# Kernel tuning notes

Hardware: AMD Instinct MI355X
Metric: run time of the kernel (lower is better)

The kernel has to match this reference:

```python
import jax, jax.numpy as jnp
import numpy as np

B, L, N_EMBD = 4, 2048, 768
N_HIDDEN, N_BINS, V, VOCAB = 32, 8, 64, 1270
TIME_BINS = np.array([0.0, 0.25, 0.5, 1.0, 2.0, 5.0, 10.0, 20.0, 40.0], dtype=np.float32)
TASK_TOKENS = np.arange(5, 5 + 19 * V, 19, dtype=np.int32)  # sorted, all > 0, < VOCAB


def setup_inputs() -> dict:
    key = jax.random.key(0)
    k0, k1, k2, k3, k4, k5 = jax.random.split(key, 6)
    # ages in years, sorted along trajectory; next-event age is slightly later
    age = jnp.sort(jax.random.uniform(k0, (B, L), dtype=jnp.float32) * 80.0, axis=-1)
    targets_age = age + jax.random.uniform(k1, (B, L), dtype=jnp.float32) * 5.0
    targets = jax.random.randint(k2, (B, L), 0, VOCAB, dtype=jnp.int32)
    h = jax.random.normal(k3, (B, L, N_EMBD), dtype=jnp.float32)
    # nn.Linear weights (stored transposed so forward is x @ W)
    W1 = jax.random.normal(k4, (N_EMBD, N_BINS * N_HIDDEN), dtype=jnp.float32) * 0.02
    W2 = jax.random.normal(k5, (N_HIDDEN, V), dtype=jnp.float32) * 0.02
    task_tokens = jnp.asarray(TASK_TOKENS)
    time_bins = jnp.asarray(TIME_BINS)
    return {"h": h, "age": age, "targets_age": targets_age, "targets": targets,
            "W1": W1, "W2": W2, "task_tokens": task_tokens, "time_bins": time_bins}


def reference(h, age, targets_age, targets, W1, W2, task_tokens, time_bins):
    # ---- time_to_event ----
    # delta_t[b, j, k] = targets_age[b, k] - age[b, j]
    delta_t = targets_age[:, None, :] - age[:, :, None]  # (B, L, L)
    # triu token map: keep target token at column k if k >= j, else 0
    jj = jnp.arange(L, dtype=jnp.int32)
    triu_mask = jj[None, :] >= jj[:, None]  # (L, L)
    targets_exp = jnp.where(triu_mask[None], targets[:, None, :], 0)  # (B, L, L)
    # token_map: task token t -> rank+1 in sorted task tokens; others -> 0
    tmap = jnp.zeros((VOCAB,), dtype=jnp.int32).at[task_tokens].set(
        jnp.arange(1, V + 1, dtype=jnp.int32))
    mapped = tmap[targets_exp]  # (B, L, L) values in [0, V]
    # scatter_reduce(amin): for each (b, j, v) find min column k with mapped == v
    seg_base = (jnp.arange(B * L, dtype=jnp.int32) * (V + 1)).reshape(B, L, 1)
    seg_ids = (seg_base + mapped).reshape(-1)
    k_idx = jnp.broadcast_to(jj[None, None, :], (B, L, L)).reshape(-1)
    tok = jax.ops.segment_min(k_idx, seg_ids, num_segments=B * L * (V + 1))
    tok = tok.reshape(B, L, V + 1)[:, :, 1:]  # drop bucket 0 -> (B, L, V)
    no_event = tok >= L  # empty segments fill with int max
    tok = jnp.minimum(tok, L - 1)
    tte = jnp.take_along_axis(delta_t, tok, axis=-1)  # (B, L, V)
    # ---- piecewise_time ----
    last_censor = targets_age[:, -1:] - age  # (B, L)
    starts, ends = time_bins[:-1], time_bins[1:]  # (N_BINS,)
    tte_e = tte[:, :, None, :]  # (B, L, 1, V)
    occur = (tte_e > starts[:, None]) & (tte_e <= ends[:, None]) & (~no_event[:, :, None, :])
    cens = jnp.clip(last_censor[:, :, None, None], 0.0, (ends - starts)[:, None])
    surv_or_event_time = jnp.where(occur, tte_e, cens)  # (B, L, N_BINS, V)
    # ---- head ----
    hh = (h @ W1).reshape(B, L, N_BINS, N_HIDDEN)
    log_lambda = jnp.einsum('blnh,hv->blnv', hh, W2)  # (B, L, N_BINS, V)
    # ---- loss ----
    ll_survival = jnp.mean(-jnp.exp(log_lambda) * surv_or_event_time)
    ll_to_event = jnp.mean(log_lambda * occur.astype(log_lambda.dtype))
    return -(ll_survival + ll_to_event)
```

## Files before the change

### kernel.cpp

```cpp
#include <hip/hip_runtime.h>
#include <hip/hip_bf16.h>

#define B_      4
#define L_      2048
#define NE_     768
#define NOUT_   256
#define NH_     32
#define NB_     8
#define V_      64
#define VOCAB_  1270
#define NC_     32
#define CS_     64
#define BM_     32
#define BK_     32
#define NT_     24
#define DEPTH_  4
#define NROWS_  8192
#define GRID_MAIN_ 256
#define INV_M_  (1.0f / 4194304.0f)
#define INF_    0x7FFFFFFF

typedef float f32x4 __attribute__((ext_vector_type(4)));
typedef short s16x8 __attribute__((ext_vector_type(8)));

__device__ __forceinline__ unsigned short f2bf(float x) {
    union { float f; unsigned u; } c; c.f = x;
    unsigned u = c.u;
    return (unsigned short)((u + 0x7fffu + ((u >> 16) & 1u)) >> 16);
}


__global__ void __launch_bounds__(256)
k_prep(const int* __restrict__ task_tokens, const float* __restrict__ W1,
       const float* __restrict__ W2, const int* __restrict__ targets,
       short* __restrict__ W1t, short* __restrict__ W2t,
       int* __restrict__ mt, int* __restrict__ firstocc, unsigned* __restrict__ cnt) {
    __shared__ float tl[64][67];
    __shared__ int   stask[V_];
    __shared__ int   smt[4][CS_];
    const int tid = threadIdx.x;

    if (blockIdx.x < 48) {
        const int tIdx = blockIdx.x;
        const int kt = (tIdx % 12) * 64;
        const int ct = (tIdx / 12) * 64;
        #pragma unroll
        for (int p = 0; p < 4; ++p) {
            int kk = (tid >> 4) + p * 16;
            int cc = (tid & 15) * 4;
            float4 v = *reinterpret_cast<const float4*>(&W1[(kt + kk) * NOUT_ + ct + cc]);
            tl[kk][cc] = v.x; tl[kk][cc + 1] = v.y; tl[kk][cc + 2] = v.z; tl[kk][cc + 3] = v.w;
        }
        __syncthreads();
        #pragma unroll
        for (int p = 0; p < 8; ++p) {
            int oc  = (tid >> 5) + p * 8;
            int ok2 = (tid & 31) * 2;
            unsigned pk = ((unsigned)f2bf(tl[ok2 + 1][oc]) << 16) | f2bf(tl[ok2][oc]);
            *reinterpret_cast<unsigned*>(&W1t[(ct + oc) * NE_ + kt + ok2]) = pk;
        }
        return;
    }
    if (blockIdx.x == 48) {
        if (tid == 0) cnt[0] = 0u;
        #pragma unroll
        for (int q = 0; q < 8; ++q) {
            int i = tid + q * 256;
            int col = i >> 5, j = i & 31;
            W2t[col * NH_ + j] = (short)f2bf(W2[j * V_ + col]);
        }
        return;
    }
    if (tid < V_) stask[tid] = task_tokens[tid];
    __syncthreads();
    const int gi = tid >> 6;
    const int v  = tid & 63;
    const int g  = (blockIdx.x - 49) * 4 + gi;
    const int b  = g >> 5, c = g & 31;
    int t = targets[b * L_ + c * CS_ + v];
    int mval = -1;
    #pragma unroll
    for (int j = 0; j < V_; ++j)
        mval = (stask[j] == t) ? j : mval;
    mt[b * L_ + c * CS_ + v] = mval;
    smt[gi][v] = mval;
    int first = INF_;
    for (int j = CS_ - 1; j >= 0; --j)
        if (smt[gi][j] == v) first = c * CS_ + j;
    firstocc[(b * NC_ + c) * V_ + v] = first;
}

__global__ void __launch_bounds__(512, 2)
k_main(const float* __restrict__ h, const float* __restrict__ age,
       const float* __restrict__ targets_age,
       const int* __restrict__ mt, const int* __restrict__ firstocc,
       const short* __restrict__ W1t, const short* __restrict__ W2t,
       const float* __restrict__ time_bins, float* __restrict__ partials,
       unsigned* __restrict__ cnt, float* __restrict__ out) {
    __shared__ __align__(16) short sA[2][BM_][40];
    __shared__ __align__(16) short sB[2][256][40];
    __shared__ __align__(16) short sW2[V_][40];
    __shared__ float stte[BM_][66];
    __shared__ int   sminI[8][V_];
    __shared__ int   smt[CS_];
    __shared__ float sage[BM_];
    __shared__ float sred[8];
    __shared__ float s2[4];
    __shared__ int   sLast;

    const int tid = threadIdx.x;
    const int w   = tid >> 6;
    const int l   = tid & 63;
    const int l15 = l & 15;
    const int l4  = l >> 4;
    const int r0  = blockIdx.x * BM_;
    const int b   = r0 >> 11;
    const int pos0 = r0 & (L_ - 1);
    const int c    = pos0 >> 6;
    const int off  = pos0 & 63;

    const int arow = tid >> 4;
    const int akc  = tid & 15;
    const int brow = tid >> 2;
    const int bch  = tid & 3;
    const float* hA  = &h[(r0 + arow) * NE_ + akc * 2];
    const short* bS0 = &W1t[brow * NE_ + bch * 8];
    const short* bS1 = &W1t[(brow + 128) * NE_ + bch * 8];

    float2 aR[DEPTH_];
    s16x8  bR0[DEPTH_], bR1[DEPTH_];
    #pragma unroll
    for (int p = 0; p < DEPTH_; ++p) {
        aR[p]  = *(const float2*)(hA + p * BK_);
        bR0[p] = *(const s16x8*)(bS0 + p * BK_);
        bR1[p] = *(const s16x8*)(bS1 + p * BK_);
    }

    if (tid < CS_)  smt[tid]  = mt[b * L_ + c * CS_ + tid];
    if (tid < BM_)  sage[tid] = age[r0 + tid];
    if (tid < 256) {
        int col = tid >> 2, ch = tid & 3;
        *(s16x8*)&sW2[col][ch * 8] = *(const s16x8*)&W2t[col * NH_ + ch * 8];
    }

    {
        int cur = INF_;
        #pragma unroll
        for (int k = 0; k < 4; ++k) {
            int cc = c + 1 + w + k * 8;
            if (cc < NC_) cur = min(cur, firstocc[(b * NC_ + cc) * V_ + l]);
        }
        sminI[w][l] = cur;
    }
    __syncthreads();

    {
        const int v  = l;
        const int rg = w;
        int cur = INF_;
        #pragma unroll
        for (int ww = 0; ww < 8; ++ww) cur = min(cur, sminI[ww][v]);
        int* stteI = (int*)stte;
        const int jmin = off + rg * 4;
        for (int j = CS_ - 1; j >= jmin; --j) {
            if (smt[j] == v) cur = c * CS_ + j;
            int br = j - off;
            if ((br >> 2) == rg) stteI[br * 66 + v] = cur;
        }
        #pragma unroll
        for (int jr = 0; jr < 4; ++jr) {
            int br  = rg * 4 + jr;
            int tok = stteI[br * 66 + v];
            float val = -1.0f;
            if (tok != INF_) val = targets_age[b * L_ + tok] - sage[br];
            stte[br][v] = val;
        }
    }

    {
        unsigned pk = ((unsigned)f2bf(aR[0].y) << 16) | f2bf(aR[0].x);
        *(unsigned*)&sA[0][arow][akc * 2] = pk;
        *(s16x8*)&sB[0][brow][bch * 8]       = bR0[0];
        *(s16x8*)&sB[0][brow + 128][bch * 8] = bR1[0];
    }
    asm volatile("s_waitcnt lgkmcnt(0)" ::: "memory");
    __builtin_amdgcn_s_barrier();
    asm volatile("" ::: "memory");

    f32x4 acc[2][2] = {};
    #pragma unroll
    for (int t = 0; t < NT_; ++t) {
        const int cur   = t & 1;
        const int slot  = t & 3;
        const int nslot = (t + 1) & 3;
        if (t < NT_ - DEPTH_) {
            aR[slot]  = *(const float2*)(hA + (t + DEPTH_) * BK_);
            bR0[slot] = *(const s16x8*)(bS0 + (t + DEPTH_) * BK_);
            bR1[slot] = *(const s16x8*)(bS1 + (t + DEPTH_) * BK_);
        }
        s16x8 af0 = *(const s16x8*)&sA[cur][l15][l4 * 8];
        s16x8 af1 = *(const s16x8*)&sA[cur][16 + l15][l4 * 8];
        s16x8 bf0 = *(const s16x8*)&sB[cur][w * 32 + l15][l4 * 8];
        s16x8 bf1 = *(const s16x8*)&sB[cur][w * 32 + 16 + l15][l4 * 8];
        acc[0][0] = __builtin_amdgcn_mfma_f32_16x16x32_bf16(af0, bf0, acc[0][0], 0, 0, 0);
        acc[0][1] = __builtin_amdgcn_mfma_f32_16x16x32_bf16(af0, bf1, acc[0][1], 0, 0, 0);
        acc[1][0] = __builtin_amdgcn_mfma_f32_16x16x32_bf16(af1, bf0, acc[1][0], 0, 0, 0);
        acc[1][1] = __builtin_amdgcn_mfma_f32_16x16x32_bf16(af1, bf1, acc[1][1], 0, 0, 0);
        if (t < NT_ - 1) {
            unsigned pk = ((unsigned)f2bf(aR[nslot].y) << 16) | f2bf(aR[nslot].x);
            *(unsigned*)&sA[cur ^ 1][arow][akc * 2] = pk;
            *(s16x8*)&sB[cur ^ 1][brow][bch * 8]       = bR0[nslot];
            *(s16x8*)&sB[cur ^ 1][brow + 128][bch * 8] = bR1[nslot];
        }
        asm volatile("s_waitcnt lgkmcnt(0)" ::: "memory");
        __builtin_amdgcn_s_barrier();
        asm volatile("" ::: "memory");
    }

    short (*sH)[BM_][40] = (short (*)[BM_][40])&sB[0][0][0];
    #pragma unroll
    for (int rf2 = 0; rf2 < 2; ++rf2)
        #pragma unroll
        for (int cfg = 0; cfg < 2; ++cfg) {
            int jj = cfg * 16 + l15;
            #pragma unroll
            for (int jr = 0; jr < 4; ++jr)
                sH[w][rf2 * 16 + l4 * 4 + jr][jj] = (short)f2bf(acc[rf2][cfg][jr]);
        }
    __syncthreads();

    const int rf = w & 1;
    const int cf = w >> 1;
    const int v  = cf * 16 + l15;
    s16x8 b2 = *(const s16x8*)&sW2[v][l4 * 8];

    float tb[NB_ + 1];
    #pragma unroll
    for (int n = 0; n <= NB_; ++n) tb[n] = time_bins[n];

    float tva[4], lcv[4];
    const float lastTA = targets_age[b * L_ + (L_ - 1)];
    #pragma unroll
    for (int jr = 0; jr < 4; ++jr) {
        int br = rf * 16 + l4 * 4 + jr;
        tva[jr] = stte[br][v];
        lcv[jr] = lastTA - sage[br];
    }

    float part = 0.0f;
    const f32x4 zero = {};
    #pragma unroll
    for (int n = 0; n < NB_; ++n) {
        s16x8 a2 = *(const s16x8*)&sH[n][rf * 16 + l15][l4 * 8];
        f32x4 c2 = __builtin_amdgcn_mfma_f32_16x16x32_bf16(a2, b2, zero, 0, 0, 0);
        float sn = tb[n], en = tb[n + 1], wn = en - sn;
        #pragma unroll
        for (int jr = 0; jr < 4; ++jr) {
            float ll = c2[jr];
            float ex = __expf(ll);
            float tv = tva[jr];
            bool occ = (tv > sn) && (tv <= en);
            float cn = fminf(fmaxf(lcv[jr], 0.0f), wn);
            part += ex * (occ ? tv : cn) - (occ ? ll : 0.0f);
        }
    }

    #pragma unroll
    for (int offs = 32; offs > 0; offs >>= 1) part += __shfl_xor(part, offs);
    if (l == 0) sred[w] = part;
    __syncthreads();
    if (tid == 0) {
        float s = 0.0f;
        #pragma unroll
        for (int i = 0; i < 8; ++i) s += sred[i];
        __hip_atomic_store(&partials[blockIdx.x], s, __ATOMIC_RELEASE, __HIP_MEMORY_SCOPE_AGENT);
        unsigned old = __hip_atomic_fetch_add(cnt, 1u, __ATOMIC_ACQ_REL, __HIP_MEMORY_SCOPE_AGENT);
        sLast = (old == GRID_MAIN_ - 1u);
    }
    __syncthreads();
    if (sLast) {
        float x = 0.0f;
        if (tid < 256)
            x = __hip_atomic_load(&partials[tid], __ATOMIC_RELAXED, __HIP_MEMORY_SCOPE_AGENT);
        #pragma unroll
        for (int o = 32; o > 0; o >>= 1) x += __shfl_xor(x, o);
        if (tid < 256 && (tid & 63) == 0) s2[tid >> 6] = x;
        __syncthreads();
        if (tid == 0) out[0] = (s2[0] + s2[1] + s2[2] + s2[3]) * INV_M_;
    }
}

extern "C" void kernel_launch(void* const* d_in, const int* in_sizes, int n_in,
                              void* d_out, int out_size, void* d_ws, size_t ws_size,
                              hipStream_t stream) {
    const float* h           = (const float*)d_in[0];
    const float* age         = (const float*)d_in[1];
    const float* targets_age = (const float*)d_in[2];
    const int*   targets     = (const int*)d_in[3];
    const float* W1          = (const float*)d_in[4];
    const float* W2          = (const float*)d_in[5];
    const int*   task_tokens = (const int*)d_in[6];
    const float* time_bins   = (const float*)d_in[7];
    float* out = (float*)d_out;

    char* ws = (char*)d_ws;
    int*      mt       = (int*)(ws + 0);
    int*      firstocc = (int*)(ws + 32768);
    short*    W1t      = (short*)(ws + 65536);
    short*    W2t      = (short*)(ws + 458752);
    float*    partials = (float*)(ws + 462848);
    unsigned* cnt      = (unsigned*)(ws + 464896);

    hipLaunchKernelGGL(k_prep, dim3(81), dim3(256), 0, stream,
                       task_tokens, W1, W2, targets, W1t, W2t, mt, firstocc, cnt);
    hipLaunchKernelGGL(k_main, dim3(GRID_MAIN_), dim3(512), 0, stream,
                       h, age, targets_age, mt, firstocc, W1t, W2t, time_bins,
                       partials, cnt, out);
}
```

Measured before the change: 33.40 us.

## Load GEMM operands directly from global into MFMA fragments, drop LDS staging

The h@W1 GEMM loop no longer stages A and B tiles through double-buffered shared memory with a register prefetch pipeline and a barrier per k-step. Each wave now loads its fragments straight from global memory, with h converted to bf16 in registers, and shared memory keeps only the small sH buffer for the second stage. This removes 24 barriers and the LDS traffic, and shrinks the LDS footprint. In exchange, each h row is loaded redundantly by all 8 waves (served from cache) and the explicit deep prefetch is gone, so latency hiding is left to the compiler and occupancy.

```diff
diff --git a/kernel.cpp b/kernel.cpp
--- a/kernel.cpp
+++ b/kernel.cpp
@@ -14,7 +14,6 @@
 #define BM_     32
 #define BK_     32
 #define NT_     24
-#define DEPTH_  4
 #define NROWS_  8192
 #define GRID_MAIN_ 256
 #define INV_M_  (1.0f / 4194304.0f)
@@ -27,6 +26,15 @@
     union { float f; unsigned u; } c; c.f = x;
     unsigned u = c.u;
     return (unsigned short)((u + 0x7fffu + ((u >> 16) & 1u)) >> 16);
+}
+__device__ __forceinline__ unsigned pk2(float lo, float hi) {
+    return ((unsigned)f2bf(hi) << 16) | (unsigned)f2bf(lo);
+}
+__device__ __forceinline__ s16x8 pack8(float4 a, float4 b) {
+    union { unsigned u[4]; s16x8 v; } r;
+    r.u[0] = pk2(a.x, a.y); r.u[1] = pk2(a.z, a.w);
+    r.u[2] = pk2(b.x, b.y); r.u[3] = pk2(b.z, b.w);
+    return r.v;
 }
 
 
@@ -97,8 +105,7 @@
        const short* __restrict__ W1t, const short* __restrict__ W2t,
        const float* __restrict__ time_bins, float* __restrict__ partials,
        unsigned* __restrict__ cnt, float* __restrict__ out) {
-    __shared__ __align__(16) short sA[2][BM_][40];
-    __shared__ __align__(16) short sB[2][256][40];
+    __shared__ __align__(16) short sH[NB_][BM_][40];
     __shared__ __align__(16) short sW2[V_][40];
     __shared__ float stte[BM_][66];
     __shared__ int   sminI[8][V_];
@@ -119,22 +126,11 @@
     const int c    = pos0 >> 6;
     const int off  = pos0 & 63;
 
-    const int arow = tid >> 4;
-    const int akc  = tid & 15;
-    const int brow = tid >> 2;
-    const int bch  = tid & 3;
-    const float* hA  = &h[(r0 + arow) * NE_ + akc * 2];
-    const short* bS0 = &W1t[brow * NE_ + bch * 8];
-    const short* bS1 = &W1t[(brow + 128) * NE_ + bch * 8];
-
-    float2 aR[DEPTH_];
-    s16x8  bR0[DEPTH_], bR1[DEPTH_];
-    #pragma unroll
-    for (int p = 0; p < DEPTH_; ++p) {
-        aR[p]  = *(const float2*)(hA + p * BK_);
-        bR0[p] = *(const s16x8*)(bS0 + p * BK_);
-        bR1[p] = *(const s16x8*)(bS1 + p * BK_);
-    }
+    const float* hA0 = &h[(r0 + l15) * NE_];
+    const float* hA1 = &h[(r0 + 16 + l15) * NE_];
+    const short* wB0 = &W1t[(w * 32 + l15) * NE_];
+    const short* wB1 = &W1t[(w * 32 + 16 + l15) * NE_];
+    const int kb = l4 * 8;
 
     if (tid < CS_)  smt[tid]  = mt[b * L_ + c * CS_ + tid];
     if (tid < BM_)  sage[tid] = age[r0 + tid];
@@ -177,47 +173,24 @@
         }
     }
 
-    {
-        unsigned pk = ((unsigned)f2bf(aR[0].y) << 16) | f2bf(aR[0].x);
-        *(unsigned*)&sA[0][arow][akc * 2] = pk;
-        *(s16x8*)&sB[0][brow][bch * 8]       = bR0[0];
-        *(s16x8*)&sB[0][brow + 128][bch * 8] = bR1[0];
-    }
-    asm volatile("s_waitcnt lgkmcnt(0)" ::: "memory");
-    __builtin_amdgcn_s_barrier();
-    asm volatile("" ::: "memory");
-
     f32x4 acc[2][2] = {};
     #pragma unroll
     for (int t = 0; t < NT_; ++t) {
-        const int cur   = t & 1;
-        const int slot  = t & 3;
-        const int nslot = (t + 1) & 3;
-        if (t < NT_ - DEPTH_) {
-            aR[slot]  = *(const float2*)(hA + (t + DEPTH_) * BK_);
-            bR0[slot] = *(const s16x8*)(bS0 + (t + DEPTH_) * BK_);
-            bR1[slot] = *(const s16x8*)(bS1 + (t + DEPTH_) * BK_);
-        }
-        s16x8 af0 = *(const s16x8*)&sA[cur][l15][l4 * 8];
-        s16x8 af1 = *(const s16x8*)&sA[cur][16 + l15][l4 * 8];
-        s16x8 bf0 = *(const s16x8*)&sB[cur][w * 32 + l15][l4 * 8];
-        s16x8 bf1 = *(const s16x8*)&sB[cur][w * 32 + 16 + l15][l4 * 8];
+        const int kk = t * BK_ + kb;
+        float4 x0 = *(const float4*)&hA0[kk];
+        float4 x1 = *(const float4*)&hA0[kk + 4];
+        float4 y0 = *(const float4*)&hA1[kk];
+        float4 y1 = *(const float4*)&hA1[kk + 4];
+        s16x8 bf0 = *(const s16x8*)&wB0[kk];
+        s16x8 bf1 = *(const s16x8*)&wB1[kk];
+        s16x8 af0 = pack8(x0, x1);
+        s16x8 af1 = pack8(y0, y1);
         acc[0][0] = __builtin_amdgcn_mfma_f32_16x16x32_bf16(af0, bf0, acc[0][0], 0, 0, 0);
         acc[0][1] = __builtin_amdgcn_mfma_f32_16x16x32_bf16(af0, bf1, acc[0][1], 0, 0, 0);
         acc[1][0] = __builtin_amdgcn_mfma_f32_16x16x32_bf16(af1, bf0, acc[1][0], 0, 0, 0);
         acc[1][1] = __builtin_amdgcn_mfma_f32_16x16x32_bf16(af1, bf1, acc[1][1], 0, 0, 0);
-        if (t < NT_ - 1) {
-            unsigned pk = ((unsigned)f2bf(aR[nslot].y) << 16) | f2bf(aR[nslot].x);
-            *(unsigned*)&sA[cur ^ 1][arow][akc * 2] = pk;
-            *(s16x8*)&sB[cur ^ 1][brow][bch * 8]       = bR0[nslot];
-            *(s16x8*)&sB[cur ^ 1][brow + 128][bch * 8] = bR1[nslot];
-        }
-        asm volatile("s_waitcnt lgkmcnt(0)" ::: "memory");
-        __builtin_amdgcn_s_barrier();
-        asm volatile("" ::: "memory");
-    }
-
-    short (*sH)[BM_][40] = (short (*)[BM_][40])&sB[0][0][0];
+    }
+
     #pragma unroll
     for (int rf2 = 0; rf2 < 2; ++rf2)
         #pragma unroll
```

New measurement: 54.25 us. 62.4% more time.

## Halve row tile to 16 and double main-kernel grid with per-bin waves

Applied to the files above, without the earlier changes.

The row tile of the fused GEMM+loss kernel drops from 32 to 16 rows, so the grid grows from 256 to 512 blocks and the launch bound now asks for 4 blocks per CU. The W1 staging is remapped so each thread loads one 16-element row chunk, and only half the threads convert h. The second stage now gives each wave one time bin and has it loop over the four V column groups, instead of splitting by row and column fragments across all bins. The intent is more blocks in flight to hide latency. In exchange, every block still streams the full W1 tile, so total W1 traffic doubles, and the tighter register budget could cause spills.

```diff
diff --git a/kernel.cpp b/kernel.cpp
--- a/kernel.cpp
+++ b/kernel.cpp
@@ -11,12 +11,12 @@
 #define VOCAB_  1270
 #define NC_     32
 #define CS_     64
-#define BM_     32
+#define BM_     16
 #define BK_     32
 #define NT_     24
 #define DEPTH_  4
 #define NROWS_  8192
-#define GRID_MAIN_ 256
+#define GRID_MAIN_ 512
 #define INV_M_  (1.0f / 4194304.0f)
 #define INF_    0x7FFFFFFF
 
@@ -90,7 +90,7 @@
     firstocc[(b * NC_ + c) * V_ + v] = first;
 }
 
-__global__ void __launch_bounds__(512, 2)
+__global__ void __launch_bounds__(512, 4)
 k_main(const float* __restrict__ h, const float* __restrict__ age,
        const float* __restrict__ targets_age,
        const int* __restrict__ mt, const int* __restrict__ firstocc,
@@ -105,7 +105,7 @@
     __shared__ int   smt[CS_];
     __shared__ float sage[BM_];
     __shared__ float sred[8];
-    __shared__ float s2[4];
+    __shared__ float s2[8];
     __shared__ int   sLast;
 
     const int tid = threadIdx.x;
@@ -121,19 +121,18 @@
 
     const int arow = tid >> 4;
     const int akc  = tid & 15;
-    const int brow = tid >> 2;
-    const int bch  = tid & 3;
-    const float* hA  = &h[(r0 + arow) * NE_ + akc * 2];
-    const short* bS0 = &W1t[brow * NE_ + bch * 8];
-    const short* bS1 = &W1t[(brow + 128) * NE_ + bch * 8];
+    const int brow = tid >> 1;
+    const int bco  = (tid & 1) * 16;
+    const float* hA = &h[(r0 + arow) * NE_ + akc * 2];
+    const short* bS = &W1t[brow * NE_ + bco];
 
     float2 aR[DEPTH_];
     s16x8  bR0[DEPTH_], bR1[DEPTH_];
     #pragma unroll
     for (int p = 0; p < DEPTH_; ++p) {
-        aR[p]  = *(const float2*)(hA + p * BK_);
-        bR0[p] = *(const s16x8*)(bS0 + p * BK_);
-        bR1[p] = *(const s16x8*)(bS1 + p * BK_);
+        if (tid < 256) aR[p] = *(const float2*)(hA + p * BK_);
+        bR0[p] = *(const s16x8*)(bS + p * BK_);
+        bR1[p] = *(const s16x8*)(bS + p * BK_ + 8);
     }
 
     if (tid < CS_)  smt[tid]  = mt[b * L_ + c * CS_ + tid];
@@ -161,15 +160,15 @@
         #pragma unroll
         for (int ww = 0; ww < 8; ++ww) cur = min(cur, sminI[ww][v]);
         int* stteI = (int*)stte;
-        const int jmin = off + rg * 4;
+        const int jmin = off + rg * 2;
         for (int j = CS_ - 1; j >= jmin; --j) {
             if (smt[j] == v) cur = c * CS_ + j;
             int br = j - off;
-            if ((br >> 2) == rg) stteI[br * 66 + v] = cur;
-        }
-        #pragma unroll
-        for (int jr = 0; jr < 4; ++jr) {
-            int br  = rg * 4 + jr;
+            if ((br >> 1) == rg) stteI[br * 66 + v] = cur;
+        }
+        #pragma unroll
+        for (int jr = 0; jr < 2; ++jr) {
+            int br  = rg * 2 + jr;
             int tok = stteI[br * 66 + v];
             float val = -1.0f;
             if (tok != INF_) val = targets_age[b * L_ + tok] - sage[br];
@@ -178,39 +177,40 @@
     }
 
     {
-        unsigned pk = ((unsigned)f2bf(aR[0].y) << 16) | f2bf(aR[0].x);
-        *(unsigned*)&sA[0][arow][akc * 2] = pk;
-        *(s16x8*)&sB[0][brow][bch * 8]       = bR0[0];
-        *(s16x8*)&sB[0][brow + 128][bch * 8] = bR1[0];
+        if (tid < 256) {
+            unsigned pk = ((unsigned)f2bf(aR[0].y) << 16) | f2bf(aR[0].x);
+            *(unsigned*)&sA[0][arow][akc * 2] = pk;
+        }
+        *(s16x8*)&sB[0][brow][bco]     = bR0[0];
+        *(s16x8*)&sB[0][brow][bco + 8] = bR1[0];
     }
     asm volatile("s_waitcnt lgkmcnt(0)" ::: "memory");
     __builtin_amdgcn_s_barrier();
     asm volatile("" ::: "memory");
 
-    f32x4 acc[2][2] = {};
+    f32x4 acc[2] = {};
     #pragma unroll
     for (int t = 0; t < NT_; ++t) {
         const int cur   = t & 1;
         const int slot  = t & 3;
         const int nslot = (t + 1) & 3;
         if (t < NT_ - DEPTH_) {
-            aR[slot]  = *(const float2*)(hA + (t + DEPTH_) * BK_);
-            bR0[slot] = *(const s16x8*)(bS0 + (t + DEPTH_) * BK_);
-            bR1[slot] = *(const s16x8*)(bS1 + (t + DEPTH_) * BK_);
-        }
-        s16x8 af0 = *(const s16x8*)&sA[cur][l15][l4 * 8];
-        s16x8 af1 = *(const s16x8*)&sA[cur][16 + l15][l4 * 8];
+            if (tid < 256) aR[slot] = *(const float2*)(hA + (t + DEPTH_) * BK_);
+            bR0[slot] = *(const s16x8*)(bS + (t + DEPTH_) * BK_);
+            bR1[slot] = *(const s16x8*)(bS + (t + DEPTH_) * BK_ + 8);
+        }
+        s16x8 af  = *(const s16x8*)&sA[cur][l15][l4 * 8];
         s16x8 bf0 = *(const s16x8*)&sB[cur][w * 32 + l15][l4 * 8];
         s16x8 bf1 = *(const s16x8*)&sB[cur][w * 32 + 16 + l15][l4 * 8];
-        acc[0][0] = __builtin_amdgcn_mfma_f32_16x16x32_bf16(af0, bf0, acc[0][0], 0, 0, 0);
-        acc[0][1] = __builtin_amdgcn_mfma_f32_16x16x32_bf16(af0, bf1, acc[0][1], 0, 0, 0);
-        acc[1][0] = __builtin_amdgcn_mfma_f32_16x16x32_bf16(af1, bf0, acc[1][0], 0, 0, 0);
-        acc[1][1] = __builtin_amdgcn_mfma_f32_16x16x32_bf16(af1, bf1, acc[1][1], 0, 0, 0);
+        acc[0] = __builtin_amdgcn_mfma_f32_16x16x32_bf16(af, bf0, acc[0], 0, 0, 0);
+        acc[1] = __builtin_amdgcn_mfma_f32_16x16x32_bf16(af, bf1, acc[1], 0, 0, 0);
         if (t < NT_ - 1) {
-            unsigned pk = ((unsigned)f2bf(aR[nslot].y) << 16) | f2bf(aR[nslot].x);
-            *(unsigned*)&sA[cur ^ 1][arow][akc * 2] = pk;
-            *(s16x8*)&sB[cur ^ 1][brow][bch * 8]       = bR0[nslot];
-            *(s16x8*)&sB[cur ^ 1][brow + 128][bch * 8] = bR1[nslot];
+            if (tid < 256) {
+                unsigned pk = ((unsigned)f2bf(aR[nslot].y) << 16) | f2bf(aR[nslot].x);
+                *(unsigned*)&sA[cur ^ 1][arow][akc * 2] = pk;
+            }
+            *(s16x8*)&sB[cur ^ 1][brow][bco]     = bR0[nslot];
+            *(s16x8*)&sB[cur ^ 1][brow][bco + 8] = bR1[nslot];
         }
         asm volatile("s_waitcnt lgkmcnt(0)" ::: "memory");
         __builtin_amdgcn_s_barrier();
@@ -219,46 +219,37 @@
 
     short (*sH)[BM_][40] = (short (*)[BM_][40])&sB[0][0][0];
     #pragma unroll
-    for (int rf2 = 0; rf2 < 2; ++rf2)
-        #pragma unroll
-        for (int cfg = 0; cfg < 2; ++cfg) {
-            int jj = cfg * 16 + l15;
-            #pragma unroll
-            for (int jr = 0; jr < 4; ++jr)
-                sH[w][rf2 * 16 + l4 * 4 + jr][jj] = (short)f2bf(acc[rf2][cfg][jr]);
-        }
-    __syncthreads();
-
-    const int rf = w & 1;
-    const int cf = w >> 1;
-    const int v  = cf * 16 + l15;
-    s16x8 b2 = *(const s16x8*)&sW2[v][l4 * 8];
-
-    float tb[NB_ + 1];
-    #pragma unroll
-    for (int n = 0; n <= NB_; ++n) tb[n] = time_bins[n];
-
-    float tva[4], lcv[4];
+    for (int cfg = 0; cfg < 2; ++cfg) {
+        int jj = cfg * 16 + l15;
+        #pragma unroll
+        for (int jr = 0; jr < 4; ++jr)
+            sH[w][l4 * 4 + jr][jj] = (short)f2bf(acc[cfg][jr]);
+    }
+    __syncthreads();
+
+    s16x8 a2 = *(const s16x8*)&sH[w][l15][l4 * 8];
+    const float sn = time_bins[w], en = time_bins[w + 1];
+    const float wn = en - sn;
     const float lastTA = targets_age[b * L_ + (L_ - 1)];
-    #pragma unroll
-    for (int jr = 0; jr < 4; ++jr) {
-        int br = rf * 16 + l4 * 4 + jr;
-        tva[jr] = stte[br][v];
-        lcv[jr] = lastTA - sage[br];
-    }
+
+    float lcv[4];
+    #pragma unroll
+    for (int jr = 0; jr < 4; ++jr)
+        lcv[jr] = lastTA - sage[l4 * 4 + jr];
 
     float part = 0.0f;
     const f32x4 zero = {};
     #pragma unroll
-    for (int n = 0; n < NB_; ++n) {
-        s16x8 a2 = *(const s16x8*)&sH[n][rf * 16 + l15][l4 * 8];
+    for (int cf = 0; cf < 4; ++cf) {
+        int v = cf * 16 + l15;
+        s16x8 b2 = *(const s16x8*)&sW2[v][l4 * 8];
         f32x4 c2 = __builtin_amdgcn_mfma_f32_16x16x32_bf16(a2, b2, zero, 0, 0, 0);
-        float sn = tb[n], en = tb[n + 1], wn = en - sn;
         #pragma unroll
         for (int jr = 0; jr < 4; ++jr) {
+            int br = l4 * 4 + jr;
             float ll = c2[jr];
             float ex = __expf(ll);
-            float tv = tva[jr];
+            float tv = stte[br][v];
             bool occ = (tv > sn) && (tv <= en);
             float cn = fminf(fmaxf(lcv[jr], 0.0f), wn);
             part += ex * (occ ? tv : cn) - (occ ? ll : 0.0f);
@@ -279,14 +270,17 @@
     }
     __syncthreads();
     if (sLast) {
-        float x = 0.0f;
-        if (tid < 256)
-            x = __hip_atomic_load(&partials[tid], __ATOMIC_RELAXED, __HIP_MEMORY_SCOPE_AGENT);
+        float x = __hip_atomic_load(&partials[tid], __ATOMIC_RELAXED, __HIP_MEMORY_SCOPE_AGENT);
         #pragma unroll
         for (int o = 32; o > 0; o >>= 1) x += __shfl_xor(x, o);
-        if (tid < 256 && (tid & 63) == 0) s2[tid >> 6] = x;
+        if (l == 0) s2[w] = x;
         __syncthreads();
-        if (tid == 0) out[0] = (s2[0] + s2[1] + s2[2] + s2[3]) * INV_M_;
+        if (tid == 0) {
+            float s = 0.0f;
+            #pragma unroll
+            for (int i = 0; i < 8; ++i) s += s2[i];
+            out[0] = s * INV_M_;
+        }
     }
 }
 
```

New measurement: 47.39 us. +41.9%, slower.

## Split fused GEMM+loss kernel into separate GEMM and loss kernels via bf16 workspace

Applied to the files above, without the earlier changes.

Splits the fused kernel into two. k_gemm computes h@W1 and writes the bf16 hidden activations to a global workspace. k_loss then handles one 64-row chunk per block: it builds the time-to-event table, runs the W2 MFMA and computes the loss terms, with each warp owning one time bin. The goal is to take the serial token-scan and tte setup off the GEMM kernel's critical path and shorten that kernel. In exchange it adds a third launch, a roughly 4 MB bf16 round trip through global memory, and a loss kernel with only 128 blocks.

```diff
diff --git a/kernel.cpp b/kernel.cpp
--- a/kernel.cpp
+++ b/kernel.cpp
@@ -16,7 +16,8 @@
 #define NT_     24
 #define DEPTH_  4
 #define NROWS_  8192
-#define GRID_MAIN_ 256
+#define GRID_GEMM_ 256
+#define GRID_LOSS_ 128
 #define INV_M_  (1.0f / 4194304.0f)
 #define INF_    0x7FFFFFFF
 
@@ -27,6 +28,9 @@
     union { float f; unsigned u; } c; c.f = x;
     unsigned u = c.u;
     return (unsigned short)((u + 0x7fffu + ((u >> 16) & 1u)) >> 16);
+}
+__device__ __forceinline__ unsigned pk2(float lo, float hi) {
+    return ((unsigned)f2bf(hi) << 16) | (unsigned)f2bf(lo);
 }
 
 
@@ -91,22 +95,10 @@
 }
 
 __global__ void __launch_bounds__(512, 2)
-k_main(const float* __restrict__ h, const float* __restrict__ age,
-       const float* __restrict__ targets_age,
-       const int* __restrict__ mt, const int* __restrict__ firstocc,
-       const short* __restrict__ W1t, const short* __restrict__ W2t,
-       const float* __restrict__ time_bins, float* __restrict__ partials,
-       unsigned* __restrict__ cnt, float* __restrict__ out) {
+k_gemm(const float* __restrict__ h, const short* __restrict__ W1t,
+       short* __restrict__ hhg) {
     __shared__ __align__(16) short sA[2][BM_][40];
     __shared__ __align__(16) short sB[2][256][40];
-    __shared__ __align__(16) short sW2[V_][40];
-    __shared__ float stte[BM_][66];
-    __shared__ int   sminI[8][V_];
-    __shared__ int   smt[CS_];
-    __shared__ float sage[BM_];
-    __shared__ float sred[8];
-    __shared__ float s2[4];
-    __shared__ int   sLast;
 
     const int tid = threadIdx.x;
     const int w   = tid >> 6;
@@ -114,10 +106,6 @@
     const int l15 = l & 15;
     const int l4  = l >> 4;
     const int r0  = blockIdx.x * BM_;
-    const int b   = r0 >> 11;
-    const int pos0 = r0 & (L_ - 1);
-    const int c    = pos0 >> 6;
-    const int off  = pos0 & 63;
 
     const int arow = tid >> 4;
     const int akc  = tid & 15;
@@ -135,51 +123,8 @@
         bR0[p] = *(const s16x8*)(bS0 + p * BK_);
         bR1[p] = *(const s16x8*)(bS1 + p * BK_);
     }
-
-    if (tid < CS_)  smt[tid]  = mt[b * L_ + c * CS_ + tid];
-    if (tid < BM_)  sage[tid] = age[r0 + tid];
-    if (tid < 256) {
-        int col = tid >> 2, ch = tid & 3;
-        *(s16x8*)&sW2[col][ch * 8] = *(const s16x8*)&W2t[col * NH_ + ch * 8];
-    }
-
     {
-        int cur = INF_;
-        #pragma unroll
-        for (int k = 0; k < 4; ++k) {
-            int cc = c + 1 + w + k * 8;
-            if (cc < NC_) cur = min(cur, firstocc[(b * NC_ + cc) * V_ + l]);
-        }
-        sminI[w][l] = cur;
-    }
-    __syncthreads();
-
-    {
-        const int v  = l;
-        const int rg = w;
-        int cur = INF_;
-        #pragma unroll
-        for (int ww = 0; ww < 8; ++ww) cur = min(cur, sminI[ww][v]);
-        int* stteI = (int*)stte;
-        const int jmin = off + rg * 4;
-        for (int j = CS_ - 1; j >= jmin; --j) {
-            if (smt[j] == v) cur = c * CS_ + j;
-            int br = j - off;
-            if ((br >> 2) == rg) stteI[br * 66 + v] = cur;
-        }
-        #pragma unroll
-        for (int jr = 0; jr < 4; ++jr) {
-            int br  = rg * 4 + jr;
-            int tok = stteI[br * 66 + v];
-            float val = -1.0f;
-            if (tok != INF_) val = targets_age[b * L_ + tok] - sage[br];
-            stte[br][v] = val;
-        }
-    }
-
-    {
-        unsigned pk = ((unsigned)f2bf(aR[0].y) << 16) | f2bf(aR[0].x);
-        *(unsigned*)&sA[0][arow][akc * 2] = pk;
+        *(unsigned*)&sA[0][arow][akc * 2] = pk2(aR[0].x, aR[0].y);
         *(s16x8*)&sB[0][brow][bch * 8]       = bR0[0];
         *(s16x8*)&sB[0][brow + 128][bch * 8] = bR1[0];
     }
@@ -207,8 +152,7 @@
         acc[1][0] = __builtin_amdgcn_mfma_f32_16x16x32_bf16(af1, bf0, acc[1][0], 0, 0, 0);
         acc[1][1] = __builtin_amdgcn_mfma_f32_16x16x32_bf16(af1, bf1, acc[1][1], 0, 0, 0);
         if (t < NT_ - 1) {
-            unsigned pk = ((unsigned)f2bf(aR[nslot].y) << 16) | f2bf(aR[nslot].x);
-            *(unsigned*)&sA[cur ^ 1][arow][akc * 2] = pk;
+            *(unsigned*)&sA[cur ^ 1][arow][akc * 2] = pk2(aR[nslot].x, aR[nslot].y);
             *(s16x8*)&sB[cur ^ 1][brow][bch * 8]       = bR0[nslot];
             *(s16x8*)&sB[cur ^ 1][brow + 128][bch * 8] = bR1[nslot];
         }
@@ -229,64 +173,131 @@
         }
     __syncthreads();
 
-    const int rf = w & 1;
-    const int cf = w >> 1;
-    const int v  = cf * 16 + l15;
-    s16x8 b2 = *(const s16x8*)&sW2[v][l4 * 8];
-
-    float tb[NB_ + 1];
-    #pragma unroll
-    for (int n = 0; n <= NB_; ++n) tb[n] = time_bins[n];
-
-    float tva[4], lcv[4];
+    {
+        const int row = tid >> 4;
+        const int c8  = (tid & 15) * 16;
+        const short* src = &sH[c8 >> 5][row][c8 & 31];
+        s16x8 v0 = *(const s16x8*)src;
+        s16x8 v1 = *(const s16x8*)(src + 8);
+        short* dst = &hhg[(r0 + row) * NOUT_ + c8];
+        *(s16x8*)dst       = v0;
+        *(s16x8*)(dst + 8) = v1;
+    }
+}
+
+__global__ void __launch_bounds__(512, 2)
+k_loss(const float* __restrict__ age, const float* __restrict__ targets_age,
+       const int* __restrict__ mt, const int* __restrict__ firstocc,
+       const short* __restrict__ hhg, const short* __restrict__ W2t,
+       const float* __restrict__ time_bins, float* __restrict__ partials,
+       unsigned* __restrict__ cnt, float* __restrict__ out) {
+    __shared__ __align__(16) short sW2[V_][40];
+    __shared__ float stte[CS_][66];
+    __shared__ int   sminI[8][V_];
+    __shared__ int   smt[CS_];
+    __shared__ float sage[CS_];
+    __shared__ float sred[8];
+    __shared__ float s2[2];
+    __shared__ int   sLast;
+
+    const int tid = threadIdx.x;
+    const int w   = tid >> 6;
+    const int l   = tid & 63;
+    const int l15 = l & 15;
+    const int l4  = l >> 4;
+    const int g   = blockIdx.x;
+    const int b   = g >> 5, c = g & 31;
+    const int r0  = g * CS_;
+
+    if (tid < CS_) { smt[tid] = mt[b * L_ + c * CS_ + tid]; sage[tid] = age[r0 + tid]; }
+    if (tid < 256) {
+        int col = tid >> 2, ch = tid & 3;
+        *(s16x8*)&sW2[col][ch * 8] = *(const s16x8*)&W2t[col * NH_ + ch * 8];
+    }
+    {
+        int cur = INF_;
+        #pragma unroll
+        for (int k = 0; k < 4; ++k) {
+            int cc = c + 1 + w + k * 8;
+            if (cc < NC_) cur = min(cur, firstocc[(b * NC_ + cc) * V_ + l]);
+        }
+        sminI[w][l] = cur;
+    }
+    __syncthreads();
+    {
+        const int v = l, rg = w;
+        int cur = INF_;
+        #pragma unroll
+        for (int ww = 0; ww < 8; ++ww) cur = min(cur, sminI[ww][v]);
+        int* stteI = (int*)stte;
+        const int jmin = rg * 8;
+        for (int j = CS_ - 1; j >= jmin; --j) {
+            if (smt[j] == v) cur = c * CS_ + j;
+            if ((j >> 3) == rg) stteI[j * 66 + v] = cur;
+        }
+        #pragma unroll
+        for (int jr = 0; jr < 8; ++jr) {
+            int j = rg * 8 + jr;
+            int tok = stteI[j * 66 + v];
+            float val = -1.0f;
+            if (tok != INF_) val = targets_age[b * L_ + tok] - sage[j];
+            stte[j][v] = val;
+        }
+    }
+    __syncthreads();
+
+    const float sn = time_bins[w], en = time_bins[w + 1];
+    const float wn = en - sn;
     const float lastTA = targets_age[b * L_ + (L_ - 1)];
-    #pragma unroll
-    for (int jr = 0; jr < 4; ++jr) {
-        int br = rf * 16 + l4 * 4 + jr;
-        tva[jr] = stte[br][v];
-        lcv[jr] = lastTA - sage[br];
-    }
-
     float part = 0.0f;
     const f32x4 zero = {};
     #pragma unroll
-    for (int n = 0; n < NB_; ++n) {
-        s16x8 a2 = *(const s16x8*)&sH[n][rf * 16 + l15][l4 * 8];
-        f32x4 c2 = __builtin_amdgcn_mfma_f32_16x16x32_bf16(a2, b2, zero, 0, 0, 0);
-        float sn = tb[n], en = tb[n + 1], wn = en - sn;
-        #pragma unroll
-        for (int jr = 0; jr < 4; ++jr) {
-            float ll = c2[jr];
-            float ex = __expf(ll);
-            float tv = tva[jr];
-            bool occ = (tv > sn) && (tv <= en);
-            float cn = fminf(fmaxf(lcv[jr], 0.0f), wn);
-            part += ex * (occ ? tv : cn) - (occ ? ll : 0.0f);
-        }
-    }
-
-    #pragma unroll
-    for (int offs = 32; offs > 0; offs >>= 1) part += __shfl_xor(part, offs);
+    for (int rg = 0; rg < 4; ++rg) {
+        s16x8 a2 = *(const s16x8*)&hhg[(r0 + rg * 16 + l15) * NOUT_ + w * 32 + l4 * 8];
+        float lcv[4];
+        #pragma unroll
+        for (int jr = 0; jr < 4; ++jr)
+            lcv[jr] = lastTA - sage[rg * 16 + l4 * 4 + jr];
+        #pragma unroll
+        for (int cf = 0; cf < 4; ++cf) {
+            int v = cf * 16 + l15;
+            s16x8 b2 = *(const s16x8*)&sW2[v][l4 * 8];
+            f32x4 c2 = __builtin_amdgcn_mfma_f32_16x16x32_bf16(a2, b2, zero, 0, 0, 0);
+            #pragma unroll
+            for (int jr = 0; jr < 4; ++jr) {
+                int row = rg * 16 + l4 * 4 + jr;
+                float ll = c2[jr];
+                float ex = __expf(ll);
+                float tv = stte[row][v];
+                bool occ = (tv > sn) && (tv <= en);
+                float cn = fminf(fmaxf(lcv[jr], 0.0f), wn);
+                part += ex * (occ ? tv : cn) - (occ ? ll : 0.0f);
+            }
+        }
+    }
+
+    #pragma unroll
+    for (int o = 32; o > 0; o >>= 1) part += __shfl_xor(part, o);
     if (l == 0) sred[w] = part;
     __syncthreads();
     if (tid == 0) {
         float s = 0.0f;
         #pragma unroll
         for (int i = 0; i < 8; ++i) s += sred[i];
-        __hip_atomic_store(&partials[blockIdx.x], s, __ATOMIC_RELEASE, __HIP_MEMORY_SCOPE_AGENT);
+        __hip_atomic_store(&partials[g], s, __ATOMIC_RELEASE, __HIP_MEMORY_SCOPE_AGENT);
         unsigned old = __hip_atomic_fetch_add(cnt, 1u, __ATOMIC_ACQ_REL, __HIP_MEMORY_SCOPE_AGENT);
-        sLast = (old == GRID_MAIN_ - 1u);
+        sLast = (old == GRID_LOSS_ - 1u);
     }
     __syncthreads();
     if (sLast) {
         float x = 0.0f;
-        if (tid < 256)
+        if (tid < GRID_LOSS_)
             x = __hip_atomic_load(&partials[tid], __ATOMIC_RELAXED, __HIP_MEMORY_SCOPE_AGENT);
         #pragma unroll
         for (int o = 32; o > 0; o >>= 1) x += __shfl_xor(x, o);
-        if (tid < 256 && (tid & 63) == 0) s2[tid >> 6] = x;
+        if (tid < GRID_LOSS_ && l == 0) s2[tid >> 6] = x;
         __syncthreads();
-        if (tid == 0) out[0] = (s2[0] + s2[1] + s2[2] + s2[3]) * INV_M_;
+        if (tid == 0) out[0] = (s2[0] + s2[1]) * INV_M_;
     }
 }
 
@@ -309,11 +320,14 @@
     short*    W1t      = (short*)(ws + 65536);
     short*    W2t      = (short*)(ws + 458752);
     float*    partials = (float*)(ws + 462848);
-    unsigned* cnt      = (unsigned*)(ws + 464896);
+    unsigned* cnt      = (unsigned*)(ws + 463872);
+    short*    hhg      = (short*)(ws + 466944);
 
     hipLaunchKernelGGL(k_prep, dim3(81), dim3(256), 0, stream,
                        task_tokens, W1, W2, targets, W1t, W2t, mt, firstocc, cnt);
-    hipLaunchKernelGGL(k_main, dim3(GRID_MAIN_), dim3(512), 0, stream,
-                       h, age, targets_age, mt, firstocc, W1t, W2t, time_bins,
+    hipLaunchKernelGGL(k_gemm, dim3(GRID_GEMM_), dim3(512), 0, stream,
+                       h, W1t, hhg);
+    hipLaunchKernelGGL(k_loss, dim3(GRID_LOSS_), dim3(512), 0, stream,
+                       age, targets_age, mt, firstocc, hhg, W2t, time_bins,
                        partials, cnt, out);
 }
```

New measurement: 35.22 us. +5.4%, slower.
